# Kernel optimization log

Measured on AMD Instinct MI355X. Metric: run time of the kernel, lower is better.

## Reference

```python
import jax, jax.numpy as jnp
import numpy as np

B, S, D, H = 4, 2048, 1024, 16
HD = D // H  # 64


def setup_inputs() -> dict:
    key = jax.random.key(0)
    k1, k2, k3 = jax.random.split(key, 3)
    scale = 1.0 / np.sqrt(D)
    return {
        "x": jax.random.normal(k1, (B, S, D), dtype=jnp.float32),
        "W_qkv": jax.random.normal(k2, (3 * D, D), dtype=jnp.float32) * scale,
        "b_qkv": jnp.zeros((3 * D,), dtype=jnp.float32),
        "W_out": jax.random.normal(k3, (D, D), dtype=jnp.float32) * scale,
        "b_out": jnp.zeros((D,), dtype=jnp.float32),
    }


def reference(x, W_qkv, b_qkv, W_out, b_out):
    b, s, d = x.shape
    # fused QKV projection: [b, s, 3d]
    qkv = jnp.einsum("bsd,ed->bse", x, W_qkv) + b_qkv
    # [b, s, H, 3*hd] -> [b, H, s, 3*hd]
    qkv = qkv.reshape(b, s, H, 3 * HD).transpose(0, 2, 1, 3)
    q, k, v = jnp.split(qkv, 3, axis=-1)  # each [b, H, s, hd]
    scaled = jnp.einsum("bhqd,bhkd->bhqk", q, k) / jnp.sqrt(jnp.float32(HD))
    attention = jax.nn.softmax(scaled, axis=-1)  # [b, H, s, s]
    values = jnp.einsum("bhqk,bhkd->bhqd", attention, v)
    values = values.transpose(0, 2, 1, 3).reshape(b, s, d)
    out = jnp.einsum("bsd,ed->bse", values, W_out) + b_out
    return out
```

## Files before the change

### kernel.cpp

```cpp
#include <hip/hip_runtime.h>

#define SEQ   2048
#define DM    1024
#define NHEAD 16
#define NBAT  4
#define NQKV  3072
#define MTOT  8192

typedef __attribute__((ext_vector_type(8))) short bf16x8;
typedef __attribute__((ext_vector_type(4))) float f32x4;
typedef __attribute__((ext_vector_type(16))) float f32x16;
typedef __attribute__((ext_vector_type(2))) unsigned int uint2v;

__device__ __forceinline__ unsigned short f2bf(float f) {
    union { float f; unsigned int u; } v; v.f = f;
    return (unsigned short)((v.u + 0x7FFFu + ((v.u >> 16) & 1u)) >> 16);
}

__device__ __forceinline__ void gl_lds16(const void* g, void* l) {
    __builtin_amdgcn_global_load_lds(
        (const __attribute__((address_space(1))) unsigned int*)(unsigned long long)g,
        (__attribute__((address_space(3))) unsigned int*)(unsigned int)(unsigned long long)l,
        16, 0, 0);
}

__global__ __launch_bounds__(256) void k_cvt_all(const float* __restrict__ x,
                                                 const float* __restrict__ wq,
                                                 const float* __restrict__ wo,
                                                 unsigned short* __restrict__ xb,
                                                 unsigned short* __restrict__ wqb,
                                                 unsigned short* __restrict__ wob) {
    int i = blockIdx.x * 256 + threadIdx.x;
    const float* s; unsigned short* d; int j;
    if (i < 2097152)      { s = x;  d = xb;  j = i; }
    else if (i < 2883584) { s = wq; d = wqb; j = i - 2097152; }
    else                  { s = wo; d = wob; j = i - 2883584; }
    float4 v = reinterpret_cast<const float4*>(s)[j];
    ushort4 o = { f2bf(v.x), f2bf(v.y), f2bf(v.z), f2bf(v.w) };
    reinterpret_cast<ushort4*>(d)[j] = o;
}

__global__ __launch_bounds__(256) void k_qkv(const unsigned short* __restrict__ X,
                                             const unsigned short* __restrict__ W,
                                             const float* __restrict__ bias,
                                             unsigned short* __restrict__ Qb,
                                             unsigned short* __restrict__ Kb,
                                             unsigned short* __restrict__ Vtb) {
    __shared__ short As[2][128 * 32];
    __shared__ short Bs[2][128 * 32];

    const int tid = threadIdx.x;
    const int lane = tid & 63;
    const int wid = tid >> 6;
    const int lr = lane & 15, g = lane >> 4;
    const int lb = (blockIdx.x & 7) * 192 + (blockIdx.x >> 3);
    const int bm = lb / (NQKV / 128);
    const int bn = lb % (NQKV / 128);
    const int m0 = bm * 128, n0 = bn * 128;
    const int wr = (wid >> 1) * 64, wc = (wid & 1) * 64;

    const f32x4 fz = {0.f, 0.f, 0.f, 0.f};
    f32x4 acc[4][4];
#pragma unroll
    for (int i = 0; i < 4; ++i)
#pragma unroll
        for (int j = 0; j < 4; ++j) acc[i][j] = fz;

    auto stage = [&](int buf, int kt) {
#pragma unroll
        for (int p = 0; p < 2; ++p) {
            int c = wid * 128 + p * 64 + lane;
            int r_ = c >> 2;
            int kc = (c & 3) ^ (r_ & 3);
            gl_lds16(X + (size_t)(m0 + r_) * DM + kt * 32 + kc * 8, &As[buf][c * 8]);
            gl_lds16(W + (size_t)(n0 + r_) * DM + kt * 32 + kc * 8, &Bs[buf][c * 8]);
        }
    };

    stage(0, 0);
    stage(1, 1);

    for (int kt = 0; kt < 32; ++kt) {
        const int cur = kt & 1;
        if (kt < 31) asm volatile("s_waitcnt vmcnt(4)" ::: "memory");
        else         asm volatile("s_waitcnt vmcnt(0)" ::: "memory");
        __builtin_amdgcn_s_barrier();

        bf16x8 a[4], b[4];
#pragma unroll
        for (int i = 0; i < 4; ++i) {
            int ra = wr + i * 16 + lr;
            a[i] = *(const bf16x8*)&As[cur][ra * 32 + ((g ^ (ra & 3)) * 8)];
            int rb = wc + i * 16 + lr;
            b[i] = *(const bf16x8*)&Bs[cur][rb * 32 + ((g ^ (rb & 3)) * 8)];
        }
        asm volatile("s_waitcnt lgkmcnt(0)" ::: "memory");
        __builtin_amdgcn_sched_barrier(0);
        __builtin_amdgcn_s_barrier();
        if (kt + 2 < 32) stage(cur, kt + 2);

#pragma unroll
        for (int i = 0; i < 4; ++i)
#pragma unroll
            for (int j = 0; j < 4; ++j)
                acc[i][j] = __builtin_amdgcn_mfma_f32_16x16x32_bf16(a[i], b[j], acc[i][j], 0, 0, 0);
    }

#pragma unroll
    for (int j = 0; j < 4; ++j) {
        const int col = n0 + wc + j * 16 + lr;
        const int h = col / 192;
        const int cc = col - h * 192;
        const int part = cc >> 6;
        const int hd = cc & 63;
        const float bv = bias[col];
#pragma unroll
        for (int i = 0; i < 4; ++i) {
            const int mbase = m0 + wr + i * 16 + g * 4;
            const int b_ = mbase >> 11;
            const int s_ = mbase & 2047;
            const int bh = b_ * NHEAD + h;
            if (part == 2) {
                ushort4 pk = { f2bf(acc[i][j][0] + bv), f2bf(acc[i][j][1] + bv),
                               f2bf(acc[i][j][2] + bv), f2bf(acc[i][j][3] + bv) };
                *(ushort4*)&Vtb[((size_t)bh * 64 + hd) * SEQ + s_] = pk;
            } else {
#pragma unroll
                for (int r = 0; r < 4; ++r) {
                    const size_t idx = ((size_t)bh * SEQ + s_ + r) * 64 + hd;
                    float v = acc[i][j][r] + bv;
                    if (part == 0) Qb[idx] = f2bf(v * (0.125f * 1.44269504f));
                    else           Kb[idx] = f2bf(v);
                }
            }
        }
    }
}

__global__ __launch_bounds__(256) void k_attn(const unsigned short* __restrict__ Qb,
                                              const unsigned short* __restrict__ Kb,
                                              const unsigned short* __restrict__ Vtb,
                                              unsigned short* __restrict__ Ob) {
    __shared__ short Ks[2][64 * 64];
    __shared__ short Vs[2][64 * 64];

    const int tid = threadIdx.x;
    const int lane = tid & 63;
    const int wid = tid >> 6;
    const int lb = (blockIdx.x & 7) * 128 + (blockIdx.x >> 3);
    const int bh = lb >> 4;
    const int qt = lb & 15;
    const int c = lane & 31;
    const int hi = lane >> 5;

    const unsigned short* Qh = Qb + (size_t)bh * SEQ * 64;
    const unsigned short* Kh = Kb + (size_t)bh * SEQ * 64;
    const unsigned short* Vh = Vtb + (size_t)bh * 64 * SEQ;

    const int q0 = qt * 128 + wid * 32;

    bf16x8 qf[4];
#pragma unroll
    for (int kc = 0; kc < 4; ++kc)
        qf[kc] = *(const bf16x8*)&Qh[(size_t)(q0 + c) * 64 + kc * 16 + hi * 8];

    f32x16 oacc[2];
    f32x16 lacc;
    f32x16 fz16;
#pragma unroll
    for (int r = 0; r < 16; ++r) { oacc[0][r] = 0.f; oacc[1][r] = 0.f; lacc[r] = 0.f; fz16[r] = 0.f; }

    auto stageK = [&](int buf, int kt) {
#pragma unroll
        for (int p = 0; p < 2; ++p) {
            int ci = wid * 128 + p * 64 + lane;
            int r_ = ci >> 3;
            int kc = (ci & 7) ^ (r_ & 7);
            gl_lds16(Kh + (size_t)(kt * 64 + r_) * 64 + kc * 8, &Ks[buf][ci * 8]);
        }
    };
    auto stageV = [&](int buf, int kt) {
#pragma unroll
        for (int p = 0; p < 2; ++p) {
            int ci = wid * 128 + p * 64 + lane;
            int r_ = ci >> 3;
            int kc = (ci & 7) ^ (r_ & 7);
            gl_lds16(Vh + (size_t)r_ * SEQ + kt * 64 + kc * 8, &Vs[buf][ci * 8]);
        }
    };

    stageK(0, 0);
    stageV(0, 0);
    __syncthreads();

    auto tile = [&](int cur, int kt) {
        if (kt + 1 < 32) { stageK(cur ^ 1, kt + 1); stageV(cur ^ 1, kt + 1); }

        f32x16 st[2];
        __builtin_amdgcn_s_setprio(1);
#pragma unroll
        for (int t = 0; t < 2; ++t) {
            const int row = t * 32 + c;
            bf16x8 kf0 = *(const bf16x8*)&Ks[cur][row * 64 + (((hi) ^ (row & 7)) * 8)];
            st[t] = __builtin_amdgcn_mfma_f32_32x32x16_bf16(kf0, qf[0], fz16, 0, 0, 0);
#pragma unroll
            for (int kc = 1; kc < 4; ++kc) {
                bf16x8 kf = *(const bf16x8*)&Ks[cur][row * 64 + (((kc * 2 + hi) ^ (row & 7)) * 8)];
                st[t] = __builtin_amdgcn_mfma_f32_32x32x16_bf16(kf, qf[kc], st[t], 0, 0, 0);
            }
        }
        __builtin_amdgcn_s_setprio(0);

        bf16x8 vf[2][4];
#pragma unroll
        for (int nb = 0; nb < 2; ++nb) {
            const int row = nb * 32 + c;
#pragma unroll
            for (int ks = 0; ks < 4; ++ks)
                vf[nb][ks] = *(const bf16x8*)&Vs[cur][row * 64 + (((ks * 2 + hi) ^ (row & 7)) * 8)];
        }

#pragma unroll
        for (int t = 0; t < 2; ++t)
#pragma unroll
            for (int r = 0; r < 16; ++r)
                st[t][r] = __builtin_amdgcn_exp2f(st[t][r]);
#pragma unroll
        for (int r = 0; r < 16; ++r)
            lacc[r] += st[0][r] + st[1][r];

        bf16x8 pa[4];
#pragma unroll
        for (int t = 0; t < 2; ++t) {
            unsigned int qd[8];
#pragma unroll
            for (int i = 0; i < 8; ++i) {
                float lo = st[t][2 * i], hg = st[t][2 * i + 1];
                unsigned int d;
                asm("v_cvt_pk_bf16_f32 %0, %1, %2" : "=v"(d) : "v"(lo), "v"(hg));
                qd[i] = d;
            }
            uint2v s02 = __builtin_amdgcn_permlane32_swap(qd[0], qd[2], false, false);
            uint2v s13 = __builtin_amdgcn_permlane32_swap(qd[1], qd[3], false, false);
            uint2v s46 = __builtin_amdgcn_permlane32_swap(qd[4], qd[6], false, false);
            uint2v s57 = __builtin_amdgcn_permlane32_swap(qd[5], qd[7], false, false);
            union { unsigned int u[4]; bf16x8 v; } pk0, pk1;
            pk0.u[0] = s02.x; pk0.u[1] = s13.x; pk0.u[2] = s02.y; pk0.u[3] = s13.y;
            pk1.u[0] = s46.x; pk1.u[1] = s57.x; pk1.u[2] = s46.y; pk1.u[3] = s57.y;
            pa[t * 2] = pk0.v;
            pa[t * 2 + 1] = pk1.v;
        }

        __builtin_amdgcn_s_setprio(1);
#pragma unroll
        for (int ks = 0; ks < 4; ++ks) {
            oacc[0] = __builtin_amdgcn_mfma_f32_32x32x16_bf16(pa[ks], vf[0][ks], oacc[0], 0, 0, 0);
            oacc[1] = __builtin_amdgcn_mfma_f32_32x32x16_bf16(pa[ks], vf[1][ks], oacc[1], 0, 0, 0);
        }
        __builtin_amdgcn_s_setprio(0);

        __syncthreads();
    };

    for (int kt = 0; kt < 32; kt += 2) { tile(0, kt); tile(1, kt + 1); }

    float lred[16];
#pragma unroll
    for (int r = 0; r < 16; ++r) lred[r] = lacc[r];
#pragma unroll
    for (int s2 = 8; s2 > 0; s2 >>= 1)
#pragma unroll
        for (int r = 0; r < s2; ++r) lred[r] += lred[r + s2];
    const float l_all = lred[0] + __shfl_xor(lred[0], 32);

    const int b_ = bh >> 4, h_ = bh & 15;
    const float linv = 1.0f / l_all;
#pragma unroll
    for (int r = 0; r < 16; ++r) {
        const int qrow = (r & 3) + 8 * (r >> 2) + 4 * hi;
        const float fr = __shfl(linv, qrow);
        const size_t mrow = (size_t)b_ * SEQ + q0 + qrow;
#pragma unroll
        for (int nb = 0; nb < 2; ++nb)
            Ob[mrow * DM + h_ * 64 + nb * 32 + c] = f2bf(oacc[nb][r] * fr);
    }
}

__global__ __launch_bounds__(256) void k_out(const unsigned short* __restrict__ A,
                                             const unsigned short* __restrict__ W,
                                             const float* __restrict__ bias,
                                             float* __restrict__ O) {
    __shared__ short As[2][128 * 32];
    __shared__ short Bs[2][128 * 32];

    const int tid = threadIdx.x;
    const int lane = tid & 63;
    const int wid = tid >> 6;
    const int lr = lane & 15, g = lane >> 4;
    const int lb = (blockIdx.x & 7) * 64 + (blockIdx.x >> 3);
    const int bm = lb / (DM / 128);
    const int bn = lb % (DM / 128);
    const int m0 = bm * 128, n0 = bn * 128;
    const int wr = (wid >> 1) * 64, wc = (wid & 1) * 64;

    const f32x4 fz = {0.f, 0.f, 0.f, 0.f};
    f32x4 acc[4][4];
#pragma unroll
    for (int i = 0; i < 4; ++i)
#pragma unroll
        for (int j = 0; j < 4; ++j) acc[i][j] = fz;

    auto stage = [&](int buf, int kt) {
#pragma unroll
        for (int p = 0; p < 2; ++p) {
            int c = wid * 128 + p * 64 + lane;
            int r_ = c >> 2;
            int kc = (c & 3) ^ (r_ & 3);
            gl_lds16(A + (size_t)(m0 + r_) * DM + kt * 32 + kc * 8, &As[buf][c * 8]);
            gl_lds16(W + (size_t)(n0 + r_) * DM + kt * 32 + kc * 8, &Bs[buf][c * 8]);
        }
    };

    stage(0, 0);
    stage(1, 1);

    for (int kt = 0; kt < 32; ++kt) {
        const int cur = kt & 1;
        if (kt < 31) asm volatile("s_waitcnt vmcnt(4)" ::: "memory");
        else         asm volatile("s_waitcnt vmcnt(0)" ::: "memory");
        __builtin_amdgcn_s_barrier();

        bf16x8 a[4], b[4];
#pragma unroll
        for (int i = 0; i < 4; ++i) {
            int ra = wr + i * 16 + lr;
            a[i] = *(const bf16x8*)&As[cur][ra * 32 + ((g ^ (ra & 3)) * 8)];
            int rb = wc + i * 16 + lr;
            b[i] = *(const bf16x8*)&Bs[cur][rb * 32 + ((g ^ (rb & 3)) * 8)];
        }
        asm volatile("s_waitcnt lgkmcnt(0)" ::: "memory");
        __builtin_amdgcn_sched_barrier(0);
        __builtin_amdgcn_s_barrier();
        if (kt + 2 < 32) stage(cur, kt + 2);

#pragma unroll
        for (int i = 0; i < 4; ++i)
#pragma unroll
            for (int j = 0; j < 4; ++j)
                acc[i][j] = __builtin_amdgcn_mfma_f32_16x16x32_bf16(a[i], b[j], acc[i][j], 0, 0, 0);
    }

#pragma unroll
    for (int j = 0; j < 4; ++j) {
        const int col = n0 + wc + j * 16 + lr;
        const float bv = bias[col];
#pragma unroll
        for (int i = 0; i < 4; ++i) {
            const int mb = m0 + wr + i * 16 + g * 4;
#pragma unroll
            for (int r = 0; r < 4; ++r)
                O[(size_t)(mb + r) * DM + col] = acc[i][j][r] + bv;
        }
    }
}

extern "C" void kernel_launch(void* const* d_in, const int* in_sizes, int n_in,
                              void* d_out, int out_size, void* d_ws, size_t ws_size,
                              hipStream_t stream) {
    const float* x    = (const float*)d_in[0];
    const float* Wqkv = (const float*)d_in[1];
    const float* bqkv = (const float*)d_in[2];
    const float* Wout = (const float*)d_in[3];
    const float* bout = (const float*)d_in[4];
    float* out = (float*)d_out;

    char* ws = (char*)d_ws;
    unsigned short* xb   = (unsigned short*)(ws);
    unsigned short* wqb  = (unsigned short*)(ws + (16u << 20));
    unsigned short* wob  = (unsigned short*)(ws + (22u << 20));
    unsigned short* Qb   = (unsigned short*)(ws + (24u << 20));
    unsigned short* Kb   = (unsigned short*)(ws + (40u << 20));
    unsigned short* Vtb  = (unsigned short*)(ws + (56u << 20));
    unsigned short* valb = (unsigned short*)(ws + (72u << 20));

    k_cvt_all<<<12288, 256, 0, stream>>>(x, Wqkv, Wout, xb, wqb, wob);
    k_qkv<<<64 * 24, 256, 0, stream>>>(xb, wqb, bqkv, Qb, Kb, Vtb);
    k_attn<<<64 * 16, 256, 0, stream>>>(Qb, Kb, Vtb, valb);
    k_out<<<64 * 8, 256, 0, stream>>>(valb, wob, bout, out);
}
```

Before: 194.8 us.

## Process two 32-row query blocks per wave to reuse K/V tiles in attention

```diff
diff --git a/kernel.cpp b/kernel.cpp
--- a/kernel.cpp
+++ b/kernel.cpp
@@ -9,6 +9,7 @@
 
 typedef __attribute__((ext_vector_type(8))) short bf16x8;
 typedef __attribute__((ext_vector_type(4))) float f32x4;
+typedef __attribute__((ext_vector_type(8))) float f32x8;
 typedef __attribute__((ext_vector_type(16))) float f32x16;
 typedef __attribute__((ext_vector_type(2))) unsigned int uint2v;
 
@@ -137,19 +138,19 @@
     }
 }
 
-__global__ __launch_bounds__(256) void k_attn(const unsigned short* __restrict__ Qb,
-                                              const unsigned short* __restrict__ Kb,
-                                              const unsigned short* __restrict__ Vtb,
-                                              unsigned short* __restrict__ Ob) {
+__global__ __launch_bounds__(256, 2) void k_attn(const unsigned short* __restrict__ Qb,
+                                                 const unsigned short* __restrict__ Kb,
+                                                 const unsigned short* __restrict__ Vtb,
+                                                 unsigned short* __restrict__ Ob) {
     __shared__ short Ks[2][64 * 64];
     __shared__ short Vs[2][64 * 64];
 
     const int tid = threadIdx.x;
     const int lane = tid & 63;
     const int wid = tid >> 6;
-    const int lb = (blockIdx.x & 7) * 128 + (blockIdx.x >> 3);
-    const int bh = lb >> 4;
-    const int qt = lb & 15;
+    const int lb = (blockIdx.x & 7) * 64 + (blockIdx.x >> 3);
+    const int bh = lb >> 3;
+    const int qt = lb & 7;
     const int c = lane & 31;
     const int hi = lane >> 5;
 
@@ -157,18 +158,26 @@
     const unsigned short* Kh = Kb + (size_t)bh * SEQ * 64;
     const unsigned short* Vh = Vtb + (size_t)bh * 64 * SEQ;
 
-    const int q0 = qt * 128 + wid * 32;
-
-    bf16x8 qf[4];
-#pragma unroll
-    for (int kc = 0; kc < 4; ++kc)
-        qf[kc] = *(const bf16x8*)&Qh[(size_t)(q0 + c) * 64 + kc * 16 + hi * 8];
-
-    f32x16 oacc[2];
-    f32x16 lacc;
+    const int q0 = qt * 256 + wid * 64;
+
+    bf16x8 qf[2][4];
+#pragma unroll
+    for (int qb = 0; qb < 2; ++qb)
+#pragma unroll
+        for (int kc = 0; kc < 4; ++kc)
+            qf[qb][kc] = *(const bf16x8*)&Qh[(size_t)(q0 + qb * 32 + c) * 64 + kc * 16 + hi * 8];
+
+    f32x16 oacc[2][2];
+    f32x8 lacc[2];
     f32x16 fz16;
 #pragma unroll
-    for (int r = 0; r < 16; ++r) { oacc[0][r] = 0.f; oacc[1][r] = 0.f; lacc[r] = 0.f; fz16[r] = 0.f; }
+    for (int r = 0; r < 16; ++r) {
+        oacc[0][0][r] = 0.f; oacc[0][1][r] = 0.f;
+        oacc[1][0][r] = 0.f; oacc[1][1][r] = 0.f;
+        fz16[r] = 0.f;
+    }
+#pragma unroll
+    for (int r = 0; r < 8; ++r) { lacc[0][r] = 0.f; lacc[1][r] = 0.f; }
 
     auto stageK = [&](int buf, int kt) {
 #pragma unroll
@@ -196,21 +205,14 @@
     auto tile = [&](int cur, int kt) {
         if (kt + 1 < 32) { stageK(cur ^ 1, kt + 1); stageV(cur ^ 1, kt + 1); }
 
-        f32x16 st[2];
-        __builtin_amdgcn_s_setprio(1);
+        bf16x8 kf[2][4];
 #pragma unroll
         for (int t = 0; t < 2; ++t) {
             const int row = t * 32 + c;
-            bf16x8 kf0 = *(const bf16x8*)&Ks[cur][row * 64 + (((hi) ^ (row & 7)) * 8)];
-            st[t] = __builtin_amdgcn_mfma_f32_32x32x16_bf16(kf0, qf[0], fz16, 0, 0, 0);
-#pragma unroll
-            for (int kc = 1; kc < 4; ++kc) {
-                bf16x8 kf = *(const bf16x8*)&Ks[cur][row * 64 + (((kc * 2 + hi) ^ (row & 7)) * 8)];
-                st[t] = __builtin_amdgcn_mfma_f32_32x32x16_bf16(kf, qf[kc], st[t], 0, 0, 0);
-            }
-        }
-        __builtin_amdgcn_s_setprio(0);
-
+#pragma unroll
+            for (int kc = 0; kc < 4; ++kc)
+                kf[t][kc] = *(const bf16x8*)&Ks[cur][row * 64 + (((kc * 2 + hi) ^ (row & 7)) * 8)];
+        }
         bf16x8 vf[2][4];
 #pragma unroll
         for (int nb = 0; nb < 2; ++nb) {
@@ -221,68 +223,84 @@
         }
 
 #pragma unroll
-        for (int t = 0; t < 2; ++t)
-#pragma unroll
-            for (int r = 0; r < 16; ++r)
-                st[t][r] = __builtin_amdgcn_exp2f(st[t][r]);
-#pragma unroll
-        for (int r = 0; r < 16; ++r)
-            lacc[r] += st[0][r] + st[1][r];
-
-        bf16x8 pa[4];
-#pragma unroll
-        for (int t = 0; t < 2; ++t) {
-            unsigned int qd[8];
-#pragma unroll
-            for (int i = 0; i < 8; ++i) {
-                float lo = st[t][2 * i], hg = st[t][2 * i + 1];
-                unsigned int d;
-                asm("v_cvt_pk_bf16_f32 %0, %1, %2" : "=v"(d) : "v"(lo), "v"(hg));
-                qd[i] = d;
+        for (int qb = 0; qb < 2; ++qb) {
+            f32x16 st[2];
+            __builtin_amdgcn_s_setprio(1);
+#pragma unroll
+            for (int t = 0; t < 2; ++t) {
+                st[t] = __builtin_amdgcn_mfma_f32_32x32x16_bf16(kf[t][0], qf[qb][0], fz16, 0, 0, 0);
+#pragma unroll
+                for (int kc = 1; kc < 4; ++kc)
+                    st[t] = __builtin_amdgcn_mfma_f32_32x32x16_bf16(kf[t][kc], qf[qb][kc], st[t], 0, 0, 0);
             }
-            uint2v s02 = __builtin_amdgcn_permlane32_swap(qd[0], qd[2], false, false);
-            uint2v s13 = __builtin_amdgcn_permlane32_swap(qd[1], qd[3], false, false);
-            uint2v s46 = __builtin_amdgcn_permlane32_swap(qd[4], qd[6], false, false);
-            uint2v s57 = __builtin_amdgcn_permlane32_swap(qd[5], qd[7], false, false);
-            union { unsigned int u[4]; bf16x8 v; } pk0, pk1;
-            pk0.u[0] = s02.x; pk0.u[1] = s13.x; pk0.u[2] = s02.y; pk0.u[3] = s13.y;
-            pk1.u[0] = s46.x; pk1.u[1] = s57.x; pk1.u[2] = s46.y; pk1.u[3] = s57.y;
-            pa[t * 2] = pk0.v;
-            pa[t * 2 + 1] = pk1.v;
-        }
-
-        __builtin_amdgcn_s_setprio(1);
-#pragma unroll
-        for (int ks = 0; ks < 4; ++ks) {
-            oacc[0] = __builtin_amdgcn_mfma_f32_32x32x16_bf16(pa[ks], vf[0][ks], oacc[0], 0, 0, 0);
-            oacc[1] = __builtin_amdgcn_mfma_f32_32x32x16_bf16(pa[ks], vf[1][ks], oacc[1], 0, 0, 0);
-        }
-        __builtin_amdgcn_s_setprio(0);
+            __builtin_amdgcn_s_setprio(0);
+
+#pragma unroll
+            for (int t = 0; t < 2; ++t)
+#pragma unroll
+                for (int r = 0; r < 16; ++r)
+                    st[t][r] = __builtin_amdgcn_exp2f(st[t][r]);
+#pragma unroll
+            for (int r = 0; r < 8; ++r)
+                lacc[qb][r] += (st[0][2 * r] + st[0][2 * r + 1]) + (st[1][2 * r] + st[1][2 * r + 1]);
+
+            bf16x8 pa[4];
+#pragma unroll
+            for (int t = 0; t < 2; ++t) {
+                unsigned int qd[8];
+#pragma unroll
+                for (int i = 0; i < 8; ++i) {
+                    float lo = st[t][2 * i], hg = st[t][2 * i + 1];
+                    unsigned int d;
+                    asm("v_cvt_pk_bf16_f32 %0, %1, %2" : "=v"(d) : "v"(lo), "v"(hg));
+                    qd[i] = d;
+                }
+                uint2v s02 = __builtin_amdgcn_permlane32_swap(qd[0], qd[2], false, false);
+                uint2v s13 = __builtin_amdgcn_permlane32_swap(qd[1], qd[3], false, false);
+                uint2v s46 = __builtin_amdgcn_permlane32_swap(qd[4], qd[6], false, false);
+                uint2v s57 = __builtin_amdgcn_permlane32_swap(qd[5], qd[7], false, false);
+                union { unsigned int u[4]; bf16x8 v; } pk0, pk1;
+                pk0.u[0] = s02.x; pk0.u[1] = s13.x; pk0.u[2] = s02.y; pk0.u[3] = s13.y;
+                pk1.u[0] = s46.x; pk1.u[1] = s57.x; pk1.u[2] = s46.y; pk1.u[3] = s57.y;
+                pa[t * 2] = pk0.v;
+                pa[t * 2 + 1] = pk1.v;
+            }
+
+            __builtin_amdgcn_s_setprio(1);
+#pragma unroll
+            for (int ks = 0; ks < 4; ++ks) {
+                oacc[qb][0] = __builtin_amdgcn_mfma_f32_32x32x16_bf16(pa[ks], vf[0][ks], oacc[qb][0], 0, 0, 0);
+                oacc[qb][1] = __builtin_amdgcn_mfma_f32_32x32x16_bf16(pa[ks], vf[1][ks], oacc[qb][1], 0, 0, 0);
+            }
+            __builtin_amdgcn_s_setprio(0);
+        }
 
         __syncthreads();
     };
 
     for (int kt = 0; kt < 32; kt += 2) { tile(0, kt); tile(1, kt + 1); }
 
-    float lred[16];
-#pragma unroll
-    for (int r = 0; r < 16; ++r) lred[r] = lacc[r];
-#pragma unroll
-    for (int s2 = 8; s2 > 0; s2 >>= 1)
-#pragma unroll
-        for (int r = 0; r < s2; ++r) lred[r] += lred[r + s2];
-    const float l_all = lred[0] + __shfl_xor(lred[0], 32);
-
     const int b_ = bh >> 4, h_ = bh & 15;
-    const float linv = 1.0f / l_all;
-#pragma unroll
-    for (int r = 0; r < 16; ++r) {
-        const int qrow = (r & 3) + 8 * (r >> 2) + 4 * hi;
-        const float fr = __shfl(linv, qrow);
-        const size_t mrow = (size_t)b_ * SEQ + q0 + qrow;
-#pragma unroll
-        for (int nb = 0; nb < 2; ++nb)
-            Ob[mrow * DM + h_ * 64 + nb * 32 + c] = f2bf(oacc[nb][r] * fr);
+#pragma unroll
+    for (int qb = 0; qb < 2; ++qb) {
+        float lred[8];
+#pragma unroll
+        for (int r = 0; r < 8; ++r) lred[r] = lacc[qb][r];
+#pragma unroll
+        for (int s2 = 4; s2 > 0; s2 >>= 1)
+#pragma unroll
+            for (int r = 0; r < s2; ++r) lred[r] += lred[r + s2];
+        const float l_all = lred[0] + __shfl_xor(lred[0], 32);
+        const float linv = 1.0f / l_all;
+#pragma unroll
+        for (int r = 0; r < 16; ++r) {
+            const int qrow = (r & 3) + 8 * (r >> 2) + 4 * hi;
+            const float fr = __shfl(linv, qrow);
+            const size_t mrow = (size_t)b_ * SEQ + q0 + qb * 32 + qrow;
+#pragma unroll
+            for (int nb = 0; nb < 2; ++nb)
+                Ob[mrow * DM + h_ * 64 + nb * 32 + c] = f2bf(oacc[qb][nb][r] * fr);
+        }
     }
 }
 
@@ -385,6 +403,6 @@
 
     k_cvt_all<<<12288, 256, 0, stream>>>(x, Wqkv, Wout, xb, wqb, wob);
     k_qkv<<<64 * 24, 256, 0, stream>>>(xb, wqb, bqkv, Qb, Kb, Vtb);
-    k_attn<<<64 * 16, 256, 0, stream>>>(Qb, Kb, Vtb, valb);
+    k_attn<<<64 * 8, 256, 0, stream>>>(Qb, Kb, Vtb, valb);
     k_out<<<64 * 8, 256, 0, stream>>>(valb, wob, bout, out);
 }
```

Measured after the change: 198.1 us. Within noise of the previous version (+1.7%).

## Fuse fp32-to-bf16 conversion of x into the QKV GEMM tile loads

Applied to the files above, without the earlier changes.

```diff
diff --git a/kernel.cpp b/kernel.cpp
--- a/kernel.cpp
+++ b/kernel.cpp
@@ -24,29 +24,26 @@
         16, 0, 0);
 }
 
-__global__ __launch_bounds__(256) void k_cvt_all(const float* __restrict__ x,
-                                                 const float* __restrict__ wq,
-                                                 const float* __restrict__ wo,
-                                                 unsigned short* __restrict__ xb,
-                                                 unsigned short* __restrict__ wqb,
-                                                 unsigned short* __restrict__ wob) {
+__global__ __launch_bounds__(256) void k_cvt_w(const float* __restrict__ wq,
+                                               const float* __restrict__ wo,
+                                               unsigned short* __restrict__ wqb,
+                                               unsigned short* __restrict__ wob) {
     int i = blockIdx.x * 256 + threadIdx.x;
     const float* s; unsigned short* d; int j;
-    if (i < 2097152)      { s = x;  d = xb;  j = i; }
-    else if (i < 2883584) { s = wq; d = wqb; j = i - 2097152; }
-    else                  { s = wo; d = wob; j = i - 2883584; }
+    if (i < 786432) { s = wq; d = wqb; j = i; }
+    else            { s = wo; d = wob; j = i - 786432; }
     float4 v = reinterpret_cast<const float4*>(s)[j];
     ushort4 o = { f2bf(v.x), f2bf(v.y), f2bf(v.z), f2bf(v.w) };
     reinterpret_cast<ushort4*>(d)[j] = o;
 }
 
-__global__ __launch_bounds__(256) void k_qkv(const unsigned short* __restrict__ X,
+__global__ __launch_bounds__(256) void k_qkv(const float* __restrict__ X,
                                              const unsigned short* __restrict__ W,
                                              const float* __restrict__ bias,
                                              unsigned short* __restrict__ Qb,
                                              unsigned short* __restrict__ Kb,
                                              unsigned short* __restrict__ Vtb) {
-    __shared__ short As[2][128 * 32];
+    __shared__ float Asf[2][128 * 32];
     __shared__ short Bs[2][128 * 32];
 
     const int tid = threadIdx.x;
@@ -68,11 +65,17 @@
 
     auto stage = [&](int buf, int kt) {
 #pragma unroll
+        for (int p = 0; p < 4; ++p) {
+            int c = p * 256 + tid;
+            int r_ = c >> 3;
+            int kc = (c & 7) ^ (r_ & 7);
+            gl_lds16(X + (size_t)(m0 + r_) * DM + kt * 32 + kc * 4, &Asf[buf][c * 4]);
+        }
+#pragma unroll
         for (int p = 0; p < 2; ++p) {
-            int c = wid * 128 + p * 64 + lane;
+            int c = p * 256 + tid;
             int r_ = c >> 2;
             int kc = (c & 3) ^ (r_ & 3);
-            gl_lds16(X + (size_t)(m0 + r_) * DM + kt * 32 + kc * 8, &As[buf][c * 8]);
             gl_lds16(W + (size_t)(n0 + r_) * DM + kt * 32 + kc * 8, &Bs[buf][c * 8]);
         }
     };
@@ -82,15 +85,18 @@
 
     for (int kt = 0; kt < 32; ++kt) {
         const int cur = kt & 1;
-        if (kt < 31) asm volatile("s_waitcnt vmcnt(4)" ::: "memory");
+        if (kt < 31) asm volatile("s_waitcnt vmcnt(6)" ::: "memory");
         else         asm volatile("s_waitcnt vmcnt(0)" ::: "memory");
         __builtin_amdgcn_s_barrier();
 
-        bf16x8 a[4], b[4];
+        float4 alo[4], ahi[4];
+        bf16x8 b[4];
 #pragma unroll
         for (int i = 0; i < 4; ++i) {
             int ra = wr + i * 16 + lr;
-            a[i] = *(const bf16x8*)&As[cur][ra * 32 + ((g ^ (ra & 3)) * 8)];
+            const float* Ar = &Asf[cur][ra * 32];
+            alo[i] = *(const float4*)&Ar[(((2 * g) ^ (ra & 7)) * 4)];
+            ahi[i] = *(const float4*)&Ar[(((2 * g + 1) ^ (ra & 7)) * 4)];
             int rb = wc + i * 16 + lr;
             b[i] = *(const bf16x8*)&Bs[cur][rb * 32 + ((g ^ (rb & 3)) * 8)];
         }
@@ -98,6 +104,17 @@
         __builtin_amdgcn_sched_barrier(0);
         __builtin_amdgcn_s_barrier();
         if (kt + 2 < 32) stage(cur, kt + 2);
+
+        bf16x8 a[4];
+#pragma unroll
+        for (int i = 0; i < 4; ++i) {
+            union { unsigned int u[4]; bf16x8 v; } av;
+            asm("v_cvt_pk_bf16_f32 %0, %1, %2" : "=v"(av.u[0]) : "v"(alo[i].x), "v"(alo[i].y));
+            asm("v_cvt_pk_bf16_f32 %0, %1, %2" : "=v"(av.u[1]) : "v"(alo[i].z), "v"(alo[i].w));
+            asm("v_cvt_pk_bf16_f32 %0, %1, %2" : "=v"(av.u[2]) : "v"(ahi[i].x), "v"(ahi[i].y));
+            asm("v_cvt_pk_bf16_f32 %0, %1, %2" : "=v"(av.u[3]) : "v"(ahi[i].z), "v"(ahi[i].w));
+            a[i] = av.v;
+        }
 
 #pragma unroll
         for (int i = 0; i < 4; ++i)
@@ -375,7 +392,6 @@
     float* out = (float*)d_out;
 
     char* ws = (char*)d_ws;
-    unsigned short* xb   = (unsigned short*)(ws);
     unsigned short* wqb  = (unsigned short*)(ws + (16u << 20));
     unsigned short* wob  = (unsigned short*)(ws + (22u << 20));
     unsigned short* Qb   = (unsigned short*)(ws + (24u << 20));
@@ -383,8 +399,8 @@
     unsigned short* Vtb  = (unsigned short*)(ws + (56u << 20));
     unsigned short* valb = (unsigned short*)(ws + (72u << 20));
 
-    k_cvt_all<<<12288, 256, 0, stream>>>(x, Wqkv, Wout, xb, wqb, wob);
-    k_qkv<<<64 * 24, 256, 0, stream>>>(xb, wqb, bqkv, Qb, Kb, Vtb);
+    k_cvt_w<<<4096, 256, 0, stream>>>(Wqkv, Wout, wqb, wob);
+    k_qkv<<<64 * 24, 256, 0, stream>>>(x, wqb, bqkv, Qb, Kb, Vtb);
     k_attn<<<64 * 16, 256, 0, stream>>>(Qb, Kb, Vtb, valb);
     k_out<<<64 * 8, 256, 0, stream>>>(valb, wob, bout, out);
 }
```

After: 201.0 us. 1.03x slower.
